# Performance work log

Hardware: AMD Instinct MI355X
Metric: run time of the kernel (lower is better)

## Reference

```python
import jax, jax.numpy as jnp
import numpy as np

NEAR = 0.0
SCENE_SCALE = 1.0
OPACITY_THRESHOLD = 0.01
EARLY_TERM = 1e-4
N_RAYS = 4096
N_SAMPLES = 256
GRID = 128
FEAT = 64
HID = 128
RGB_HID = 64


def mip360_contract(c):
    # Mip-NeRF 360 scene contraction; safe norm avoids NaN grads in the unused branch.
    norm = jnp.linalg.norm(c, axis=-1, keepdims=True)
    safe = jnp.maximum(norm, 1e-12)
    return jnp.where(norm <= 1.0, c, (2.0 - 1.0 / safe) * c / safe) / 2.0


def unbounded_stepping(near, uniform_range, n):
    ts = jnp.linspace(0.0, 1.0 - 1.0 / (n + 2), n + 1)
    ts = jnp.where(ts < 0.5, 2.0 * ts, 1.0 / (2.0 - 2.0 * ts)) * uniform_range + near
    return ts[:-1], ts[1:] - ts[:-1]


def grid_sample_3d(grid, coords):
    # torch F.grid_sample bilinear, align_corners=False, zeros padding.
    # grid [D,H,W]; coords [...,3] = (x,y,z) with x->W, y->H, z->D, in [-1,1].
    D, H, W = grid.shape
    x, y, z = coords[..., 0], coords[..., 1], coords[..., 2]
    ix = ((x + 1.0) * W - 1.0) * 0.5
    iy = ((y + 1.0) * H - 1.0) * 0.5
    iz = ((z + 1.0) * D - 1.0) * 0.5
    ix0, iy0, iz0 = jnp.floor(ix), jnp.floor(iy), jnp.floor(iz)
    fx, fy, fz = ix - ix0, iy - iy0, iz - iz0
    out = jnp.zeros(x.shape, grid.dtype)
    for dz in (0, 1):
        for dy in (0, 1):
            for dx in (0, 1):
                cx, cy, cz = ix0 + dx, iy0 + dy, iz0 + dz
                w = (fx if dx else 1.0 - fx) * (fy if dy else 1.0 - fy) * (fz if dz else 1.0 - fz)
                valid = (cx >= 0) & (cx < W) & (cy >= 0) & (cy < H) & (cz >= 0) & (cz < D)
                g = grid[jnp.clip(cz, 0, D - 1).astype(jnp.int32),
                         jnp.clip(cy, 0, H - 1).astype(jnp.int32),
                         jnp.clip(cx, 0, W - 1).astype(jnp.int32)]
                out = out + jnp.where(valid, w * g, 0.0)
    return out


def setup_inputs() -> dict:
    key = jax.random.key(0)
    ks = jax.random.split(key, 8)
    rays_o = jax.random.normal(ks[0], (N_RAYS, 3), jnp.float32) * 0.3
    rd = jax.random.normal(ks[1], (N_RAYS, 3), jnp.float32)
    rays_d = rd / jnp.linalg.norm(rd, axis=-1, keepdims=True)
    grid = jax.random.uniform(ks[2], (GRID, GRID, GRID), jnp.float32)
    lin = lambda k, fan_in, shape: jax.random.normal(k, shape, jnp.float32) / np.sqrt(fan_in).astype(np.float32)
    return dict(
        rays_o=rays_o, rays_d=rays_d, grid=grid,
        f_w1=lin(ks[3], 3, (3, HID)), f_b1=jnp.zeros((HID,), jnp.float32),
        f_w2=lin(ks[4], HID, (HID, FEAT)), f_b2=jnp.zeros((FEAT,), jnp.float32),
        s_w=lin(ks[5], FEAT, (FEAT, 1)), s_b=jnp.zeros((1,), jnp.float32),
        r_w1=lin(ks[6], FEAT + 3, (FEAT + 3, RGB_HID)), r_b1=jnp.zeros((RGB_HID,), jnp.float32),
        r_w2=lin(ks[7], RGB_HID, (RGB_HID, 3)), r_b2=jnp.zeros((3,), jnp.float32),
        n_samples=N_SAMPLES,
    )


def reference(rays_o, rays_d, grid, f_w1, f_b1, f_w2, f_b2, s_w, s_b, r_w1, r_b1, r_w2, r_b2, n_samples):
    n_rays = rays_o.shape[0]
    t, dist = unbounded_stepping(NEAR, SCENE_SCALE, n_samples)               # [S], [S]
    samples = rays_o[:, None, :] + rays_d[:, None, :] * t[None, :, None]     # [R,S,3]
    samples = mip360_contract(samples)
    occ = grid_sample_3d(grid, samples)                                      # [R,S]
    mask = occ > OPACITY_THRESHOLD
    # feature module (dense compute, masked write as in samples_features[mask] = ...)
    feat = jax.nn.relu(samples @ f_w1 + f_b1) @ f_w2 + f_b2                  # [R,S,F]
    feat = jnp.where(mask[..., None], feat, 0.0)
    sigma = jnp.where(mask, jax.nn.softplus(feat @ s_w + s_b)[..., 0], 0.0)  # [R,S]
    a = -sigma * dist[None, :]
    trans = jnp.concatenate(
        [jnp.ones((n_rays, 1), a.dtype), jnp.exp(jnp.cumsum(a, axis=1))[:, :-1]], axis=1)
    weights = trans * (1.0 - jnp.exp(a))                                     # [R,S]
    mask2 = mask & (trans > EARLY_TERM)
    dirs = jnp.broadcast_to(rays_d[:, None, :], samples.shape)
    h = jax.nn.relu(jnp.concatenate([feat, dirs], axis=-1) @ r_w1 + r_b1)
    rgb = jax.nn.sigmoid(h @ r_w2 + r_b2) * weights[..., None]
    rgb = jnp.where(mask2[..., None], rgb, 0.0)
    return rgb.sum(axis=1)                                                   # [R,3]
```

## Files before the change

### kernel.cpp

```cpp
#include <hip/hip_runtime.h>
#include <math.h>
#include <stdint.h>

#define S    256
#define GN   128

typedef __attribute__((ext_vector_type(8))) short  short8;
typedef __attribute__((ext_vector_type(4))) float  floatx4;

#define WS_BHI 0
#define WS_RW1 16384
#define WS_B2S 24576
#define WS_WS2 24592
#define WS_W1P 25104

__device__ __forceinline__ unsigned short bf16_rtne(float f) {
    uint32_t u = __builtin_bit_cast(uint32_t, f);
    uint32_t r = (u + 0x7fffu + ((u >> 16) & 1u)) >> 16;
    return (unsigned short)r;
}
__device__ __forceinline__ unsigned short bf16_rhu(float f) {
    return (unsigned short)((__builtin_bit_cast(uint32_t, f) + 0x8000u) >> 16);
}

__global__ __launch_bounds__(256)
void nerf_prep(const float* __restrict__ f_w1, const float* __restrict__ f_b1,
               const float* __restrict__ f_w2, const float* __restrict__ f_b2,
               const float* __restrict__ s_w,  const float* __restrict__ s_b,
               const float* __restrict__ r_w1, unsigned char* __restrict__ ws)
{
    const int tid = threadIdx.x;
    if (tid < 128) {
        float acc = 0.0f;
        for (int n = 0; n < 64; ++n) acc += f_w2[tid * 64 + n] * s_w[n];
        ((float*)(ws + WS_WS2))[tid] = acc;
    } else if (tid == 128) {
        float acc = s_b[0];
        for (int n = 0; n < 64; ++n) acc += f_b2[n] * s_w[n];
        *(float*)(ws + WS_B2S) = acc;
    }
    {
        float* w1pk = (float*)(ws + WS_W1P);
        for (int k = tid; k < 128; k += 256) {
            w1pk[k * 4 + 0] = f_w1[k];
            w1pk[k * 4 + 1] = f_w1[128 + k];
            w1pk[k * 4 + 2] = f_w1[256 + k];
            w1pk[k * 4 + 3] = f_b1[k];
        }
    }

    unsigned short* bhi = (unsigned short*)(ws + WS_BHI);
    for (int i = tid; i < 8192; i += 256) {
        int j = i & 7, L = (i >> 3) & 63, g = i >> 9;
        int tn = g & 3, kc = g >> 2;
        int q = L >> 4, cc = L & 15;
        int k = kc * 32 + q * 8 + j;
        bhi[i] = bf16_rtne(f_w2[k * 64 + tn * 16 + cc]);
    }
    unsigned short* rw = (unsigned short*)(ws + WS_RW1);
    for (int i = tid; i < 4096; i += 256) {
        int j = i & 7, L = (i >> 3) & 63, g = i >> 9;
        int tn = g & 3, ks = g >> 2;
        int q = L >> 4, cc = L & 15;
        int k = ks * 32 + q * 8 + j;
        rw[i] = bf16_rtne(r_w1[k * 64 + tn * 16 + cc]);
    }
}

__global__ __launch_bounds__(256, 3)
void nerf_mfma(const float* __restrict__ rays_o,
               const float* __restrict__ rays_d,
               const float* __restrict__ grid,
               const float* __restrict__ f_b2,
               const float* __restrict__ r_w1,
               const float* __restrict__ r_b1,
               const float* __restrict__ r_w2,
               const float* __restrict__ r_b2,
               const unsigned char* __restrict__ ws,
               float* __restrict__ out)
{
    __shared__ unsigned short fh[256 * 64];
    __shared__ float w1p[512];
    __shared__ float ws2L[128];
    __shared__ float aLds[S];
    __shared__ float maskLds[S];
    __shared__ float distLds[S];
    __shared__ float sWaveSum[4];
    __shared__ float sPart[4][3];

    const int tid   = threadIdx.x;
    const int ray   = blockIdx.x;
    const int lane  = tid & 63;
    const int wv    = tid >> 6;
    const int q     = lane >> 4;
    const int c     = lane & 15;
    const int mbase = wv * 64;

    if (tid < 128) {
        ((float4*)w1p)[tid] = ((const float4*)(ws + WS_W1P))[tid];
        ws2L[tid] = ((const float*)(ws + WS_WS2))[tid];
    }

    const float stop = 1.0f - 1.0f / (float)(S + 2);
    const float step = stop / (float)S;
    float u0 = (float)tid * step;
    float u1 = (float)(tid + 1) * step;
    float t    = (u0 < 0.5f) ? 2.0f * u0 : 1.0f / (2.0f - 2.0f * u0);
    float tn_  = (u1 < 0.5f) ? 2.0f * u1 : 1.0f / (2.0f - 2.0f * u1);
    float dist = tn_ - t;

    float ox = rays_o[ray * 3 + 0], oy = rays_o[ray * 3 + 1], oz = rays_o[ray * 3 + 2];
    float dxv = rays_d[ray * 3 + 0], dyv = rays_d[ray * 3 + 1], dzv = rays_d[ray * 3 + 2];

    float px = ox + dxv * t, py = oy + dyv * t, pz = oz + dzv * t;
    float nrm = sqrtf(px * px + py * py + pz * pz);
    float scale = (nrm <= 1.0f) ? 0.5f : (2.0f - 1.0f / nrm) / nrm * 0.5f;
    float cx = px * scale, cy = py * scale, cz = pz * scale;

    float ix = ((cx + 1.0f) * (float)GN - 1.0f) * 0.5f;
    float iy = ((cy + 1.0f) * (float)GN - 1.0f) * 0.5f;
    float iz = ((cz + 1.0f) * (float)GN - 1.0f) * 0.5f;
    float fx0 = floorf(ix), fy0 = floorf(iy), fz0 = floorf(iz);
    float fx = ix - fx0, fy = iy - fy0, fz = iz - fz0;
    int x0 = (int)fx0, y0 = (int)fy0, z0 = (int)fz0;

    float occ = 0.0f;
    #pragma unroll
    for (int dzc = 0; dzc < 2; ++dzc)
    #pragma unroll
    for (int dyc = 0; dyc < 2; ++dyc)
    #pragma unroll
    for (int dxc = 0; dxc < 2; ++dxc) {
        int xc = x0 + dxc, yc = y0 + dyc, zc = z0 + dzc;
        float w = (dxc ? fx : 1.0f - fx) * (dyc ? fy : 1.0f - fy) * (dzc ? fz : 1.0f - fz);
        if (xc >= 0 && xc < GN && yc >= 0 && yc < GN && zc >= 0 && zc < GN)
            occ += w * grid[(zc * GN + yc) * GN + xc];
    }
    bool maskA = occ > 0.01f;
    maskLds[tid] = maskA ? 1.0f : 0.0f;
    distLds[tid] = dist;

    float cxs[4], cys[4], czs[4];
    #pragma unroll
    for (int tm = 0; tm < 4; ++tm) {
        int src = tm * 16 + c;
        cxs[tm] = __shfl(cx, src, 64);
        cys[tm] = __shfl(cy, src, 64);
        czs[tm] = __shfl(cz, src, 64);
    }
    __syncthreads();

    floatx4 facc[4][4];
    {
        float b2v[4];
        #pragma unroll
        for (int tn = 0; tn < 4; ++tn) b2v[tn] = f_b2[tn * 16 + c];
        #pragma unroll
        for (int tm = 0; tm < 4; ++tm)
            #pragma unroll
            for (int tn = 0; tn < 4; ++tn) {
                floatx4 v; v[0] = b2v[tn]; v[1] = b2v[tn]; v[2] = b2v[tn]; v[3] = b2v[tn];
                facc[tm][tn] = v;
            }
    }
    float sig[4] = {0.0f, 0.0f, 0.0f, 0.0f};

    const unsigned short* __restrict__ bhiP = (const unsigned short*)(ws + WS_BHI);

    #pragma unroll 1
    for (int kc = 0; kc < 4; ++kc) {
        const int k0 = kc * 32 + q * 8;
        const float4* __restrict__ w1q = (const float4*)&w1p[k0 * 4];
        float ws2r[8];
        *(float4*)(ws2r)     = *(const float4*)&ws2L[k0];
        *(float4*)(ws2r + 4) = *(const float4*)&ws2L[k0 + 4];

        short8 Ah[4];
        #pragma unroll
        for (int j = 0; j < 8; ++j) {
            float4 w = w1q[j];
            #pragma unroll
            for (int tm = 0; tm < 4; ++tm) {
                float h = w.w + cxs[tm] * w.x + cys[tm] * w.y + czs[tm] * w.z;
                h = fmaxf(h, 0.0f);
                sig[tm] += h * ws2r[j];
                Ah[tm][j] = (short)bf16_rhu(h);
            }
        }
        const int bbase = (kc * 4) * 512 + lane * 8;
        #pragma unroll
        for (int tn = 0; tn < 4; ++tn) {
            short8 bh = *(const short8*)(bhiP + bbase + tn * 512);
            #pragma unroll
            for (int tm = 0; tm < 4; ++tm)
                facc[tm][tn] = __builtin_amdgcn_mfma_f32_16x16x32_bf16(Ah[tm], bh, facc[tm][tn], 0, 0, 0);
        }
    }

    #pragma unroll
    for (int tm = 0; tm < 4; ++tm)
        #pragma unroll
        for (int tn = 0; tn < 4; ++tn)
            #pragma unroll
            for (int reg = 0; reg < 4; ++reg) {
                int m = mbase + tm * 16 + q * 4 + reg;
                int n = tn * 16 + c;
                int idx = m * 64 + (((n >> 3) ^ (m & 7)) << 3) + (n & 7);
                fh[idx] = bf16_rhu(facc[tm][tn][reg]);
            }

    {
        #pragma unroll
        for (int tm = 0; tm < 4; ++tm) {
            sig[tm] += __shfl_xor(sig[tm], 16);
            sig[tm] += __shfl_xor(sig[tm], 32);
        }
        float b2s = *(const float*)(ws + WS_B2S);
        if (q == 0) {
            #pragma unroll
            for (int tm = 0; tm < 4; ++tm) {
                int m = mbase + tm * 16 + c;
                float sa = sig[tm] + b2s;
                float sg = (maskLds[m] > 0.5f)
                         ? (fmaxf(sa, 0.0f) + __logf(1.0f + __expf(-fabsf(sa)))) : 0.0f;
                aLds[m] = -sg * distLds[m];
            }
        }
    }
    __builtin_amdgcn_wave_barrier();

    float av = aLds[tid];
    float v = av;
    #pragma unroll
    for (int off = 1; off < 64; off <<= 1) {
        float u2 = __shfl_up(v, off);
        if (lane >= off) v += u2;
    }
    if (lane == 63) sWaveSum[wv] = v;
    __syncthreads();
    float basev = 0.0f;
    #pragma unroll
    for (int w = 0; w < 4; ++w) basev += (w < wv) ? sWaveSum[w] : 0.0f;
    float excl = __shfl_up(v, 1);
    if (lane == 0) excl = 0.0f;
    float cum    = basev + excl;
    float trans  = __expf(cum);
    float weight = trans * (1.0f - __expf(av));
    bool  mask2  = maskA && (trans > 1e-4f);

    float hd[4];
    #pragma unroll
    for (int tn = 0; tn < 4; ++tn) {
        int n = tn * 16 + c;
        hd[tn] = r_b1[n] + dxv * r_w1[64 * 64 + n] + dyv * r_w1[65 * 64 + n] + dzv * r_w1[66 * 64 + n];
    }

    short8 afr[4][2];
    #pragma unroll
    for (int tm = 0; tm < 4; ++tm)
        #pragma unroll
        for (int ks = 0; ks < 2; ++ks) {
            int m = mbase + tm * 16 + c;
            int gl = ks * 4 + q;
            afr[tm][ks] = *(const short8*)&fh[m * 64 + ((gl ^ (m & 7)) << 3)];
        }

    floatx4 hacc[4][4];
    #pragma unroll
    for (int tm = 0; tm < 4; ++tm)
        #pragma unroll
        for (int tn = 0; tn < 4; ++tn) {
            floatx4 z; z[0] = 0.0f; z[1] = 0.0f; z[2] = 0.0f; z[3] = 0.0f;
            hacc[tm][tn] = z;
        }
    const unsigned short* __restrict__ rwP = (const unsigned short*)(ws + WS_RW1);
    #pragma unroll
    for (int ks = 0; ks < 2; ++ks)
        #pragma unroll
        for (int tn = 0; tn < 4; ++tn) {
            short8 rb = *(const short8*)(rwP + ((ks * 4 + tn) * 64 + lane) * 8);
            #pragma unroll
            for (int tm = 0; tm < 4; ++tm)
                hacc[tm][tn] = __builtin_amdgcn_mfma_f32_16x16x32_bf16(afr[tm][ks], rb, hacc[tm][tn], 0, 0, 0);
        }

    __builtin_amdgcn_wave_barrier();
    #pragma unroll
    for (int tm = 0; tm < 4; ++tm)
        #pragma unroll
        for (int tn = 0; tn < 4; ++tn)
            #pragma unroll
            for (int reg = 0; reg < 4; ++reg) {
                int m = mbase + tm * 16 + q * 4 + reg;
                int n = tn * 16 + c;
                float hv = fmaxf(hacc[tm][tn][reg] + hd[tn], 0.0f);
                int idx = m * 64 + (((n >> 3) ^ (m & 7)) << 3) + (n & 7);
                fh[idx] = bf16_rhu(hv);
            }
    __builtin_amdgcn_wave_barrier();

    float o0 = r_b2[0], o1 = r_b2[1], o2 = r_b2[2];
    const uint32_t* __restrict__ fr = (const uint32_t*)fh;
    #pragma unroll
    for (int gl = 0; gl < 8; ++gl) {
        int pg = gl ^ (tid & 7);
        uint4 pk = *(const uint4*)(fr + tid * 32 + pg * 4);
        uint32_t pw[4] = {pk.x, pk.y, pk.z, pk.w};
        #pragma unroll
        for (int tt = 0; tt < 4; ++tt) {
            float h0 = __builtin_bit_cast(float, pw[tt] << 16);
            float h1 = __builtin_bit_cast(float, pw[tt] & 0xffff0000u);
            int k = gl * 8 + 2 * tt;
            o0 += h0 * r_w2[k * 3 + 0] + h1 * r_w2[k * 3 + 3];
            o1 += h0 * r_w2[k * 3 + 1] + h1 * r_w2[k * 3 + 4];
            o2 += h0 * r_w2[k * 3 + 2] + h1 * r_w2[k * 3 + 5];
        }
    }
    float r = 0.0f, g = 0.0f, b = 0.0f;
    if (mask2) {
        r = weight / (1.0f + __expf(-o0));
        g = weight / (1.0f + __expf(-o1));
        b = weight / (1.0f + __expf(-o2));
    }

    #pragma unroll
    for (int off = 32; off > 0; off >>= 1) {
        r += __shfl_down(r, off);
        g += __shfl_down(g, off);
        b += __shfl_down(b, off);
    }
    if (lane == 0) { sPart[wv][0] = r; sPart[wv][1] = g; sPart[wv][2] = b; }
    __syncthreads();
    if (tid == 0) {
        out[ray * 3 + 0] = sPart[0][0] + sPart[1][0] + sPart[2][0] + sPart[3][0];
        out[ray * 3 + 1] = sPart[0][1] + sPart[1][1] + sPart[2][1] + sPart[3][1];
        out[ray * 3 + 2] = sPart[0][2] + sPart[1][2] + sPart[2][2] + sPart[3][2];
    }
}

extern "C" void kernel_launch(void* const* d_in, const int* in_sizes, int n_in,
                              void* d_out, int out_size, void* d_ws, size_t ws_size,
                              hipStream_t stream) {
    const int n_rays = in_sizes[0] / 3;
    nerf_prep<<<1, 256, 0, stream>>>(
        (const float*)d_in[3], (const float*)d_in[4], (const float*)d_in[5],
        (const float*)d_in[6], (const float*)d_in[7], (const float*)d_in[8],
        (const float*)d_in[9], (unsigned char*)d_ws);
    nerf_mfma<<<n_rays, 256, 0, stream>>>(
        (const float*)d_in[0],  (const float*)d_in[1],  (const float*)d_in[2],
        (const float*)d_in[6],  (const float*)d_in[9],  (const float*)d_in[10],
        (const float*)d_in[11], (const float*)d_in[12],
        (const unsigned char*)d_ws, (float*)d_out);
}
```

Measured before the change: 190.4 us.

## Fuse weight-prep kernel into main kernel and stage MFMA weights in LDS

Removes the separate single-block prep kernel and has every ray block convert f_w2 and r_w1 to bf16 MFMA fragment layout directly into shared memory, and compute the folded sigma weights itself. B-fragment loads then come from LDS instead of the global workspace, and one launch plus its serialization are saved. In exchange, each of the thousands of blocks repeats the full weight conversion and the dot products. LDS use also grows by the extra r_w1 buffer, with an added barrier before the f_w2 staging area is reused.

```diff
diff --git a/kernel.cpp b/kernel.cpp
--- a/kernel.cpp
+++ b/kernel.cpp
@@ -7,12 +7,6 @@
 
 typedef __attribute__((ext_vector_type(8))) short  short8;
 typedef __attribute__((ext_vector_type(4))) float  floatx4;
-
-#define WS_BHI 0
-#define WS_RW1 16384
-#define WS_B2S 24576
-#define WS_WS2 24592
-#define WS_W1P 25104
 
 __device__ __forceinline__ unsigned short bf16_rtne(float f) {
     uint32_t u = __builtin_bit_cast(uint32_t, f);
@@ -23,65 +17,27 @@
     return (unsigned short)((__builtin_bit_cast(uint32_t, f) + 0x8000u) >> 16);
 }
 
-__global__ __launch_bounds__(256)
-void nerf_prep(const float* __restrict__ f_w1, const float* __restrict__ f_b1,
-               const float* __restrict__ f_w2, const float* __restrict__ f_b2,
-               const float* __restrict__ s_w,  const float* __restrict__ s_b,
-               const float* __restrict__ r_w1, unsigned char* __restrict__ ws)
-{
-    const int tid = threadIdx.x;
-    if (tid < 128) {
-        float acc = 0.0f;
-        for (int n = 0; n < 64; ++n) acc += f_w2[tid * 64 + n] * s_w[n];
-        ((float*)(ws + WS_WS2))[tid] = acc;
-    } else if (tid == 128) {
-        float acc = s_b[0];
-        for (int n = 0; n < 64; ++n) acc += f_b2[n] * s_w[n];
-        *(float*)(ws + WS_B2S) = acc;
-    }
-    {
-        float* w1pk = (float*)(ws + WS_W1P);
-        for (int k = tid; k < 128; k += 256) {
-            w1pk[k * 4 + 0] = f_w1[k];
-            w1pk[k * 4 + 1] = f_w1[128 + k];
-            w1pk[k * 4 + 2] = f_w1[256 + k];
-            w1pk[k * 4 + 3] = f_b1[k];
-        }
-    }
-
-    unsigned short* bhi = (unsigned short*)(ws + WS_BHI);
-    for (int i = tid; i < 8192; i += 256) {
-        int j = i & 7, L = (i >> 3) & 63, g = i >> 9;
-        int tn = g & 3, kc = g >> 2;
-        int q = L >> 4, cc = L & 15;
-        int k = kc * 32 + q * 8 + j;
-        bhi[i] = bf16_rtne(f_w2[k * 64 + tn * 16 + cc]);
-    }
-    unsigned short* rw = (unsigned short*)(ws + WS_RW1);
-    for (int i = tid; i < 4096; i += 256) {
-        int j = i & 7, L = (i >> 3) & 63, g = i >> 9;
-        int tn = g & 3, ks = g >> 2;
-        int q = L >> 4, cc = L & 15;
-        int k = ks * 32 + q * 8 + j;
-        rw[i] = bf16_rtne(r_w1[k * 64 + tn * 16 + cc]);
-    }
-}
-
 __global__ __launch_bounds__(256, 3)
-void nerf_mfma(const float* __restrict__ rays_o,
-               const float* __restrict__ rays_d,
-               const float* __restrict__ grid,
-               const float* __restrict__ f_b2,
-               const float* __restrict__ r_w1,
-               const float* __restrict__ r_b1,
-               const float* __restrict__ r_w2,
-               const float* __restrict__ r_b2,
-               const unsigned char* __restrict__ ws,
-               float* __restrict__ out)
+void nerf_fused(const float* __restrict__ rays_o,
+                const float* __restrict__ rays_d,
+                const float* __restrict__ grid,
+                const float* __restrict__ f_w1,
+                const float* __restrict__ f_b1,
+                const float* __restrict__ f_w2,
+                const float* __restrict__ f_b2,
+                const float* __restrict__ s_w,
+                const float* __restrict__ s_b,
+                const float* __restrict__ r_w1,
+                const float* __restrict__ r_b1,
+                const float* __restrict__ r_w2,
+                const float* __restrict__ r_b2,
+                float* __restrict__ out)
 {
     __shared__ unsigned short fh[256 * 64];
+    __shared__ unsigned short rwL[4096];
     __shared__ float w1p[512];
     __shared__ float ws2L[128];
+    __shared__ float b2sL;
     __shared__ float aLds[S];
     __shared__ float maskLds[S];
     __shared__ float distLds[S];
@@ -96,9 +52,29 @@
     const int c     = lane & 15;
     const int mbase = wv * 64;
 
+    for (int i = tid; i < 8192; i += 256) {
+        int k = i >> 6, n = i & 63;
+        int pos = (((k >> 5) * 4 + (n >> 4)) * 64 + ((k >> 3) & 3) * 16 + (n & 15)) * 8 + (k & 7);
+        fh[pos] = bf16_rtne(f_w2[i]);
+    }
+    for (int i = tid; i < 4096; i += 256) {
+        int k = i >> 6, n = i & 63;
+        int pos = (((k >> 5) * 4 + (n >> 4)) * 64 + ((k >> 3) & 3) * 16 + (n & 15)) * 8 + (k & 7);
+        rwL[pos] = bf16_rtne(r_w1[i]);
+    }
     if (tid < 128) {
-        ((float4*)w1p)[tid] = ((const float4*)(ws + WS_W1P))[tid];
-        ws2L[tid] = ((const float*)(ws + WS_WS2))[tid];
+        w1p[tid * 4 + 0] = f_w1[tid];
+        w1p[tid * 4 + 1] = f_w1[128 + tid];
+        w1p[tid * 4 + 2] = f_w1[256 + tid];
+        w1p[tid * 4 + 3] = f_b1[tid];
+        const float* __restrict__ row = f_w2 + tid * 64;
+        float acc = 0.0f;
+        for (int n = 0; n < 64; ++n) acc += row[n] * s_w[n];
+        ws2L[tid] = acc;
+    } else if (tid == 128) {
+        float acc = s_b[0];
+        for (int n = 0; n < 64; ++n) acc += f_b2[n] * s_w[n];
+        b2sL = acc;
     }
 
     const float stop = 1.0f - 1.0f / (float)(S + 2);
@@ -150,7 +126,7 @@
     }
     __syncthreads();
 
-    floatx4 facc[4][4];
+    floatx4 acc[4][4];
     {
         float b2v[4];
         #pragma unroll
@@ -160,12 +136,10 @@
             #pragma unroll
             for (int tn = 0; tn < 4; ++tn) {
                 floatx4 v; v[0] = b2v[tn]; v[1] = b2v[tn]; v[2] = b2v[tn]; v[3] = b2v[tn];
-                facc[tm][tn] = v;
+                acc[tm][tn] = v;
             }
     }
     float sig[4] = {0.0f, 0.0f, 0.0f, 0.0f};
-
-    const unsigned short* __restrict__ bhiP = (const unsigned short*)(ws + WS_BHI);
 
     #pragma unroll 1
     for (int kc = 0; kc < 4; ++kc) {
@@ -187,15 +161,16 @@
                 Ah[tm][j] = (short)bf16_rhu(h);
             }
         }
-        const int bbase = (kc * 4) * 512 + lane * 8;
+        const int bbase = kc * 2048 + lane * 8;
         #pragma unroll
         for (int tn = 0; tn < 4; ++tn) {
-            short8 bh = *(const short8*)(bhiP + bbase + tn * 512);
+            short8 bh = *(const short8*)&fh[bbase + tn * 512];
             #pragma unroll
             for (int tm = 0; tm < 4; ++tm)
-                facc[tm][tn] = __builtin_amdgcn_mfma_f32_16x16x32_bf16(Ah[tm], bh, facc[tm][tn], 0, 0, 0);
-        }
-    }
+                acc[tm][tn] = __builtin_amdgcn_mfma_f32_16x16x32_bf16(Ah[tm], bh, acc[tm][tn], 0, 0, 0);
+        }
+    }
+    __syncthreads();
 
     #pragma unroll
     for (int tm = 0; tm < 4; ++tm)
@@ -206,7 +181,7 @@
                 int m = mbase + tm * 16 + q * 4 + reg;
                 int n = tn * 16 + c;
                 int idx = m * 64 + (((n >> 3) ^ (m & 7)) << 3) + (n & 7);
-                fh[idx] = bf16_rhu(facc[tm][tn][reg]);
+                fh[idx] = bf16_rhu(acc[tm][tn][reg]);
             }
 
     {
@@ -215,7 +190,7 @@
             sig[tm] += __shfl_xor(sig[tm], 16);
             sig[tm] += __shfl_xor(sig[tm], 32);
         }
-        float b2s = *(const float*)(ws + WS_B2S);
+        float b2s = b2sL;
         if (q == 0) {
             #pragma unroll
             for (int tm = 0; tm < 4; ++tm) {
@@ -265,23 +240,21 @@
             afr[tm][ks] = *(const short8*)&fh[m * 64 + ((gl ^ (m & 7)) << 3)];
         }
 
-    floatx4 hacc[4][4];
     #pragma unroll
     for (int tm = 0; tm < 4; ++tm)
         #pragma unroll
         for (int tn = 0; tn < 4; ++tn) {
             floatx4 z; z[0] = 0.0f; z[1] = 0.0f; z[2] = 0.0f; z[3] = 0.0f;
-            hacc[tm][tn] = z;
-        }
-    const unsigned short* __restrict__ rwP = (const unsigned short*)(ws + WS_RW1);
+            acc[tm][tn] = z;
+        }
     #pragma unroll
     for (int ks = 0; ks < 2; ++ks)
         #pragma unroll
         for (int tn = 0; tn < 4; ++tn) {
-            short8 rb = *(const short8*)(rwP + ((ks * 4 + tn) * 64 + lane) * 8);
+            short8 rb = *(const short8*)&rwL[((ks * 4 + tn) * 64 + lane) * 8];
             #pragma unroll
             for (int tm = 0; tm < 4; ++tm)
-                hacc[tm][tn] = __builtin_amdgcn_mfma_f32_16x16x32_bf16(afr[tm][ks], rb, hacc[tm][tn], 0, 0, 0);
+                acc[tm][tn] = __builtin_amdgcn_mfma_f32_16x16x32_bf16(afr[tm][ks], rb, acc[tm][tn], 0, 0, 0);
         }
 
     __builtin_amdgcn_wave_barrier();
@@ -293,7 +266,7 @@
             for (int reg = 0; reg < 4; ++reg) {
                 int m = mbase + tm * 16 + q * 4 + reg;
                 int n = tn * 16 + c;
-                float hv = fmaxf(hacc[tm][tn][reg] + hd[tn], 0.0f);
+                float hv = fmaxf(acc[tm][tn][reg] + hd[tn], 0.0f);
                 int idx = m * 64 + (((n >> 3) ^ (m & 7)) << 3) + (n & 7);
                 fh[idx] = bf16_rhu(hv);
             }
@@ -342,13 +315,10 @@
                               void* d_out, int out_size, void* d_ws, size_t ws_size,
                               hipStream_t stream) {
     const int n_rays = in_sizes[0] / 3;
-    nerf_prep<<<1, 256, 0, stream>>>(
-        (const float*)d_in[3], (const float*)d_in[4], (const float*)d_in[5],
-        (const float*)d_in[6], (const float*)d_in[7], (const float*)d_in[8],
-        (const float*)d_in[9], (unsigned char*)d_ws);
-    nerf_mfma<<<n_rays, 256, 0, stream>>>(
+    nerf_fused<<<n_rays, 256, 0, stream>>>(
         (const float*)d_in[0],  (const float*)d_in[1],  (const float*)d_in[2],
-        (const float*)d_in[6],  (const float*)d_in[9],  (const float*)d_in[10],
-        (const float*)d_in[11], (const float*)d_in[12],
-        (const unsigned char*)d_ws, (float*)d_out);
+        (const float*)d_in[3],  (const float*)d_in[4],  (const float*)d_in[5],
+        (const float*)d_in[6],  (const float*)d_in[7],  (const float*)d_in[8],
+        (const float*)d_in[9],  (const float*)d_in[10], (const float*)d_in[11],
+        (const float*)d_in[12], (float*)d_out);
 }
```

After: 197.1 us. 1.04x slower.
